# Kernel optimization log

Measured on AMD Instinct MI355X. Metric: run time of the kernel, lower is better.

The kernel has to match this reference:

```python
import jax, jax.numpy as jnp
import numpy as np


def setup_inputs() -> dict:
    key = jax.random.key(0)
    k1, k2 = jax.random.split(key)
    n, c, h, w = 8, 2048, 64, 64
    out_c = 512
    fea = jax.random.normal(k1, (n, c, h, w), dtype=jnp.float32)
    # Conv2d weight [out, in, kh=1, kw=9]; kaiming-ish scale
    W = jax.random.normal(k2, (out_c, c, 1, 9), dtype=jnp.float32) * 0.02
    b = jnp.zeros((out_c,), dtype=jnp.float32)
    return {"fea": fea, "W": W, "b": b}


def reference(fea, W, b):
    # Original module (stride=1 path): for each width column i, take the
    # [n,c,h,1] slice, run Conv2d(kernel=(1,9), pad=(0,4)) + ReLU, concat on w.
    # For a width-1 input, only the CENTER kernel tap (kw index 4) overlaps
    # real data; all other taps see zero padding. Hence each column output is
    # ReLU(W[:,:,0,4] @ column + b), and the concat over columns is exactly a
    # pointwise (1x1) conv over the full feature map with the center tap.
    Wc = W[:, :, 0, 4]  # [out_c, in_c]
    out = jnp.einsum('nchw,oc->nohw', fea, Wc) + b[None, :, None, None]
    return jax.nn.relu(out)
```

## Files before the change

### kernel.cpp

```cpp
#include <hip/hip_runtime.h>
#include <hip/hip_bf16.h>

typedef __bf16 bf16x4 __attribute__((ext_vector_type(4)));
typedef __bf16 bf16x8 __attribute__((ext_vector_type(8)));
typedef float floatx4 __attribute__((ext_vector_type(4)));

#define KDIM 2048
#define MDIM 512
#define HWDIM 4096
#define BN 64
#define BK 32
#define NITER (KDIM / BK)

__global__ void extract_w_kernel(const float* __restrict__ W, __bf16* __restrict__ Wc) {
  int e = (blockIdx.x * 256 + threadIdx.x) * 4;
  bf16x4 h;
#pragma unroll
  for (int j = 0; j < 4; ++j) h[j] = (__bf16)W[(size_t)(e + j) * 9 + 4];
  *(bf16x4*)(Wc + e) = h;
}

__global__ __launch_bounds__(512, 4) void conv1x1_kernel(
    const float* __restrict__ fea, const __bf16* __restrict__ Wc,
    const float* __restrict__ bias, float* __restrict__ out) {
  __shared__ __align__(16) __bf16 Bs[2][BN * BK];

  const int t    = threadIdx.x;
  const int wave = t >> 6;
  const int lane = t & 63;
  const int l15  = lane & 15;
  const int quad = lane >> 4;
  const int wm   = wave * 64;

  const int img = blockIdx.x >> 6;
  const int nb  = blockIdx.x & 63;

  const float* feaN = fea + (size_t)img * KDIM * HWDIM + (size_t)nb * BN;
  float*       outN = out + (size_t)img * MDIM * HWDIM + (size_t)nb * BN;

  const int hw   = lane;
  const int kg   = wave;
  const int boff = hw * BK + (kg ^ ((hw >> 1) & 7)) * 4;
  const float* bsrc = feaN + (size_t)kg * 4 * HWDIM + hw;

  const __bf16* aptr = Wc + (size_t)(wm + l15) * KDIM + quad * 8;

  floatx4 acc[4][4];
#pragma unroll
  for (int i = 0; i < 4; ++i)
#pragma unroll
    for (int j = 0; j < 4; ++j) acc[i][j] = (floatx4){0.f, 0.f, 0.f, 0.f};

  {
    float v[4];
#pragma unroll
    for (int j = 0; j < 4; ++j) v[j] = bsrc[(size_t)j * HWDIM];
    bf16x4 h;
#pragma unroll
    for (int j = 0; j < 4; ++j) h[j] = (__bf16)v[j];
    *(bf16x4*)&Bs[0][boff] = h;
  }
  __syncthreads();

  for (int iter = 0; iter < NITER; ++iter) {
    const int cur = iter & 1;

    float vn[4];
    if (iter + 1 < NITER) {
      const float* p = bsrc + (size_t)(iter + 1) * BK * HWDIM;
#pragma unroll
      for (int j = 0; j < 4; ++j) vn[j] = p[(size_t)j * HWDIM];
    }

    bf16x8 af[4];
    const __bf16* ap = aptr + iter * BK;
#pragma unroll
    for (int mt = 0; mt < 4; ++mt)
      af[mt] = *(const bf16x8*)(ap + (size_t)mt * 16 * KDIM);

    bf16x8 bfr[4];
#pragma unroll
    for (int nt = 0; nt < 4; ++nt) {
      const int n  = nt * 16 + l15;
      const int sw = (n >> 1) & 7;
      const __bf16* row = &Bs[cur][n * BK];
      union { bf16x8 v8; bf16x4 v4[2]; } u;
      u.v4[0] = *(const bf16x4*)(row + ((quad * 2) ^ sw) * 4);
      u.v4[1] = *(const bf16x4*)(row + ((quad * 2 + 1) ^ sw) * 4);
      bfr[nt] = u.v8;
    }

#pragma unroll
    for (int mt = 0; mt < 4; ++mt)
#pragma unroll
      for (int nt = 0; nt < 4; ++nt)
        acc[mt][nt] = __builtin_amdgcn_mfma_f32_16x16x32_bf16(af[mt], bfr[nt], acc[mt][nt], 0, 0, 0);

    if (iter + 1 < NITER) {
      bf16x4 hn;
#pragma unroll
      for (int j = 0; j < 4; ++j) hn[j] = (__bf16)vn[j];
      *(bf16x4*)&Bs[cur ^ 1][boff] = hn;
    }
    __syncthreads();
  }

#pragma unroll
  for (int mt = 0; mt < 4; ++mt) {
    const int o0 = wm + mt * 16 + quad * 4;
    const float4 bv = *(const float4*)(bias + o0);
    const float bvr[4] = {bv.x, bv.y, bv.z, bv.w};
#pragma unroll
    for (int r = 0; r < 4; ++r) {
      const size_t ro = (size_t)(o0 + r) * HWDIM;
#pragma unroll
      for (int nt = 0; nt < 4; ++nt) {
        float x = acc[mt][nt][r] + bvr[r];
        outN[ro + nt * 16 + l15] = x > 0.f ? x : 0.f;
      }
    }
  }
}

extern "C" void kernel_launch(void* const* d_in, const int* in_sizes, int n_in,
                              void* d_out, int out_size, void* d_ws, size_t ws_size,
                              hipStream_t stream) {
  const float* fea  = (const float*)d_in[0];
  const float* W    = (const float*)d_in[1];
  const float* bias = (const float*)d_in[2];
  float* out = (float*)d_out;
  __bf16* Wc = (__bf16*)d_ws;

  hipLaunchKernelGGL(extract_w_kernel, dim3(1024), dim3(256), 0, stream, W, Wc);
  hipLaunchKernelGGL(conv1x1_kernel, dim3(512), dim3(512), 0, stream, fea, Wc, bias, out);
}
```

Before: 495.4 us.

## Stage B tile with half the waves using two-deep register prefetch and 16B LDS ops

Only waves 0-3 now load the fp32 feature tile, each thread fetching 8 k-values instead of 4. Loads run two iterations ahead in a register double buffer, and the loop is unrolled by two so buffer indices stay static. The bf16 conversion and LDS store now happen at the start of the iteration rather than after the MFMAs. LDS writes and reads become single 16-byte accesses with a new 4-way XOR swizzle, replacing paired 8-byte reads. The aim is to hide global load latency and cut LDS instruction count. In exchange, the staging waves carry an extra 16 floats in registers, and load work is unevenly split across waves.

```diff
diff --git a/kernel.cpp b/kernel.cpp
--- a/kernel.cpp
+++ b/kernel.cpp
@@ -38,72 +38,71 @@
   const float* feaN = fea + (size_t)img * KDIM * HWDIM + (size_t)nb * BN;
   float*       outN = out + (size_t)img * MDIM * HWDIM + (size_t)nb * BN;
 
-  const int hw   = lane;
-  const int kg   = wave;
-  const int boff = hw * BK + (kg ^ ((hw >> 1) & 7)) * 4;
-  const float* bsrc = feaN + (size_t)kg * 4 * HWDIM + hw;
+  const bool stager = (wave < 4);
+  const int  hw   = lane;
+  const int  g    = wave & 3;
+  const int  boff = hw * BK + ((g ^ ((hw >> 1) & 3)) * 8);
+  const float* bsrc = feaN + (size_t)g * 8 * HWDIM + hw;
 
   const __bf16* aptr = Wc + (size_t)(wm + l15) * KDIM + quad * 8;
 
+  float bpf[2][8];
   floatx4 acc[4][4];
 #pragma unroll
   for (int i = 0; i < 4; ++i)
 #pragma unroll
     for (int j = 0; j < 4; ++j) acc[i][j] = (floatx4){0.f, 0.f, 0.f, 0.f};
 
-  {
-    float v[4];
+  if (stager) {
 #pragma unroll
-    for (int j = 0; j < 4; ++j) v[j] = bsrc[(size_t)j * HWDIM];
-    bf16x4 h;
+    for (int j = 0; j < 8; ++j) bpf[0][j] = bsrc[(size_t)j * HWDIM];
 #pragma unroll
-    for (int j = 0; j < 4; ++j) h[j] = (__bf16)v[j];
-    *(bf16x4*)&Bs[0][boff] = h;
+    for (int j = 0; j < 8; ++j) bpf[1][j] = bsrc[(size_t)(BK + j) * HWDIM];
+    bf16x8 h0;
+#pragma unroll
+    for (int j = 0; j < 8; ++j) h0[j] = (__bf16)bpf[0][j];
+    *(bf16x8*)&Bs[0][boff] = h0;
   }
   __syncthreads();
 
-  for (int iter = 0; iter < NITER; ++iter) {
-    const int cur = iter & 1;
+#define KBODY(I, CUR)                                                          \
+  {                                                                            \
+    const int i_ = (I);                                                        \
+    bf16x8 af[4];                                                              \
+    const __bf16* ap = aptr + i_ * BK;                                         \
+    _Pragma("unroll")                                                          \
+    for (int mt = 0; mt < 4; ++mt)                                             \
+      af[mt] = *(const bf16x8*)(ap + (size_t)mt * 16 * KDIM);                  \
+    if (stager && i_ + 1 < NITER) {                                            \
+      bf16x8 hn;                                                               \
+      _Pragma("unroll")                                                        \
+      for (int j = 0; j < 8; ++j) hn[j] = (__bf16)bpf[(CUR) ^ 1][j];           \
+      *(bf16x8*)&Bs[(CUR) ^ 1][boff] = hn;                                     \
+    }                                                                          \
+    if (stager && i_ + 2 < NITER) {                                            \
+      const float* p = bsrc + (size_t)(i_ + 2) * BK * HWDIM;                   \
+      _Pragma("unroll")                                                        \
+      for (int j = 0; j < 8; ++j) bpf[(CUR)][j] = p[(size_t)j * HWDIM];        \
+    }                                                                          \
+    _Pragma("unroll")                                                          \
+    for (int nt = 0; nt < 4; ++nt) {                                           \
+      const int n_ = nt * 16 + l15;                                            \
+      const bf16x8 bfr =                                                       \
+          *(const bf16x8*)&Bs[(CUR)][n_ * BK + ((quad ^ ((n_ >> 1) & 3)) * 8)];\
+      _Pragma("unroll")                                                        \
+      for (int mt = 0; mt < 4; ++mt)                                           \
+        acc[mt][nt] = __builtin_amdgcn_mfma_f32_16x16x32_bf16(af[mt], bfr,     \
+                                                              acc[mt][nt],    \
+                                                              0, 0, 0);       \
+    }                                                                          \
+    __syncthreads();                                                           \
+  }
 
-    float vn[4];
-    if (iter + 1 < NITER) {
-      const float* p = bsrc + (size_t)(iter + 1) * BK * HWDIM;
-#pragma unroll
-      for (int j = 0; j < 4; ++j) vn[j] = p[(size_t)j * HWDIM];
-    }
-
-    bf16x8 af[4];
-    const __bf16* ap = aptr + iter * BK;
-#pragma unroll
-    for (int mt = 0; mt < 4; ++mt)
-      af[mt] = *(const bf16x8*)(ap + (size_t)mt * 16 * KDIM);
-
-    bf16x8 bfr[4];
-#pragma unroll
-    for (int nt = 0; nt < 4; ++nt) {
-      const int n  = nt * 16 + l15;
-      const int sw = (n >> 1) & 7;
-      const __bf16* row = &Bs[cur][n * BK];
-      union { bf16x8 v8; bf16x4 v4[2]; } u;
-      u.v4[0] = *(const bf16x4*)(row + ((quad * 2) ^ sw) * 4);
-      u.v4[1] = *(const bf16x4*)(row + ((quad * 2 + 1) ^ sw) * 4);
-      bfr[nt] = u.v8;
-    }
-
-#pragma unroll
-    for (int mt = 0; mt < 4; ++mt)
-#pragma unroll
-      for (int nt = 0; nt < 4; ++nt)
-        acc[mt][nt] = __builtin_amdgcn_mfma_f32_16x16x32_bf16(af[mt], bfr[nt], acc[mt][nt], 0, 0, 0);
-
-    if (iter + 1 < NITER) {
-      bf16x4 hn;
-#pragma unroll
-      for (int j = 0; j < 4; ++j) hn[j] = (__bf16)vn[j];
-      *(bf16x4*)&Bs[cur ^ 1][boff] = hn;
-    }
-    __syncthreads();
+  for (int i = 0; i < NITER; i += 2) {
+    KBODY(i, 0)
+    KBODY(i + 1, 1)
   }
+#undef KBODY
 
 #pragma unroll
   for (int mt = 0; mt < 4; ++mt) {
```

Result: faster. 484.0 us (-2.3%).
